# Optimization experiments

Measured on AMD Instinct MI355X. Metric: run time of the kernel, lower is better.

Reference implementation:

```python
import jax, jax.numpy as jnp
import numpy as np

S, B, V = 128, 64, 32000
EH, EO, H, O = 512, 512, 1024, 1024
THRESH = 1e-06


def _thresh(x):
    # nn.Threshold(1e-6, 0): x if x > 1e-6 else 0
    return jnp.where(x > THRESH, x, 0.0)


def setup_inputs() -> dict:
    key = jax.random.key(0)
    ks = jax.random.split(key, 12)
    ids = jax.random.randint(ks[0], (S, B), 0, V, dtype=jnp.int32)
    s = 0.02
    return {
        "ids": ids,
        "W1": jax.random.normal(ks[1], (EH, V), jnp.float32) * s,
        "b1": jax.random.normal(ks[2], (EH,), jnp.float32) * s,
        "W2": jax.random.normal(ks[3], (EO, EH), jnp.float32) * s,
        "b2": jax.random.normal(ks[4], (EO,), jnp.float32) * s,
        "W_ih": jax.random.normal(ks[5], (3 * H, EO), jnp.float32) * s,
        "b_ih": jax.random.normal(ks[6], (3 * H,), jnp.float32) * s,
        "W_hh": jax.random.normal(ks[7], (3 * H, H), jnp.float32) * s,
        "b_hh": jax.random.normal(ks[8], (3 * H,), jnp.float32) * s,
        "W_out": jax.random.normal(ks[9], (O, H), jnp.float32) * s,
        "b_out": jax.random.normal(ks[10], (O,), jnp.float32) * s,
    }


def reference(ids, W1, b1, W2, b2, W_ih, b_ih, W_hh, b_hh, W_out, b_out):
    # one_hot(ids, V) @ W1.T + b1 == exact gather of W1 columns (sum of zeros is exact)
    emb = _thresh(jnp.take(W1.T, ids, axis=0) + b1)            # [S, B, EH]
    x = _thresh(jnp.einsum('sbe,oe->sbo', emb, W2) + b2)       # [S, B, EO]
    # Precompute all input-gate projections in one GEMM
    xW = jnp.einsum('sbe,ge->sbg', x, W_ih) + b_ih             # [S, B, 3H]

    def step(h, xw):
        gh = h @ W_hh.T + b_hh                                 # [B, 3H]
        xr, xz, xn = jnp.split(xw, 3, axis=-1)
        hr, hz, hn = jnp.split(gh, 3, axis=-1)
        r = jax.nn.sigmoid(xr + hr)
        z = jax.nn.sigmoid(xz + hz)
        n = jnp.tanh(xn + r * hn)
        h_new = (1.0 - z) * n + z * h
        return h_new, None

    h0 = jnp.zeros((B, H), dtype=x.dtype)
    hT, _ = jax.lax.scan(step, h0, xW)                         # [B, H]
    # Dropout is identity in inference; final Linear
    out = hT @ W_out.T + b_out                                 # [B, O]
    return out[None]                                           # [1, B, O] (h_n layout)
```

## Files before the change

### kernel.cpp

```cpp
#include <hip/hip_runtime.h>
#include <stdint.h>
#include <stddef.h>

#define S_LEN 128
#define B_SZ  64
#define V_SZ  32000
#define EH    512
#define EO    512
#define H_SZ  1024
#define O_SZ  1024
#define G3    3072

typedef __attribute__((ext_vector_type(8))) short short8;
typedef __attribute__((ext_vector_type(4))) float floatx4;
typedef __attribute__((ext_vector_type(8))) unsigned short ushortx8;
typedef __attribute__((ext_vector_type(4))) unsigned uintx4;

__device__ __forceinline__ unsigned short f2bf(float f) {
  unsigned u = __builtin_bit_cast(unsigned, f);
  u += 0x7FFFu + ((u >> 16) & 1u);
  return (unsigned short)(u >> 16);
}
__device__ __forceinline__ float bf2f(unsigned short h) {
  unsigned u = ((unsigned)h) << 16;
  return __builtin_bit_cast(float, u);
}

__device__ __forceinline__ void gld_lds16(const void* g, void* l) {
  __builtin_amdgcn_global_load_lds((const __attribute__((address_space(1))) void*)g,
                                   (__attribute__((address_space(3))) void*)l, 16, 0, 0);
}

__global__ __launch_bounds__(256) void cvt2_bf16(const float* __restrict__ a,
                                                 const float* __restrict__ b,
                                                 unsigned short* __restrict__ out) {
  const int na4 = (EO * EH) / 4;
  int i = blockIdx.x * 256 + threadIdx.x;
  const float* src;
  int off;
  if (i < na4) { src = a; off = i; }
  else         { src = b; off = i - na4; }
  float4 v = ((const float4*)src)[off];
  ushort4 o;
  o.x = f2bf(v.x); o.y = f2bf(v.y); o.z = f2bf(v.z); o.w = f2bf(v.w);
  ((ushort4*)out)[i] = o;
}

__global__ __launch_bounds__(256) void transpose_w1_bf16(const float* __restrict__ W1,
                                                         unsigned short* __restrict__ W1T) {
  __shared__ unsigned short tile[64][72];
  int t = threadIdx.x;
  int v0 = blockIdx.x * 64;
  int e0 = blockIdx.y * 64;
  for (int i = 0; i < 4; ++i) {
    int e = (t >> 4) + i * 16;
    int v = (t & 15) * 4;
    float4 w = *(const float4*)&W1[(size_t)(e0 + e) * V_SZ + v0 + v];
    tile[v + 0][e] = f2bf(w.x);
    tile[v + 1][e] = f2bf(w.y);
    tile[v + 2][e] = f2bf(w.z);
    tile[v + 3][e] = f2bf(w.w);
  }
  __syncthreads();
  for (int i = 0; i < 2; ++i) {
    int v = (t >> 3) + i * 32;
    int e = (t & 7) * 8;
    ushortx8 o;
    for (int j = 0; j < 8; ++j) o[j] = tile[v][e + j];
    *(ushortx8*)&W1T[(size_t)(v0 + v) * EH + e0 + e] = o;
  }
}

__global__ __launch_bounds__(256) void gather_emb(const int* __restrict__ ids,
                                                  const unsigned short* __restrict__ W1T,
                                                  const float* __restrict__ b1,
                                                  unsigned short* __restrict__ emb) {
  int t = threadIdx.x;
  int tok = blockIdx.x * 4 + (t >> 6);
  int lane = t & 63;
  int id = ids[tok];
  ushortx8 w = *(const ushortx8*)&W1T[(size_t)id * EH + lane * 8];
  float4 blo = *(const float4*)&b1[lane * 8];
  float4 bhi = *(const float4*)&b1[lane * 8 + 4];
  float bv[8] = {blo.x, blo.y, blo.z, blo.w, bhi.x, bhi.y, bhi.z, bhi.w};
  ushortx8 o;
  for (int j = 0; j < 8; ++j) {
    float x = bf2f(w[j]) + bv[j];
    x = (x > 1e-6f) ? x : 0.0f;
    o[j] = f2bf(x);
  }
  *(ushortx8*)&emb[(size_t)tok * EH + lane * 8] = o;
}

template <int ACT, int OUT_BF16>
__global__ __launch_bounds__(256) void gemm_bt(const unsigned short* __restrict__ A,
                                               const unsigned short* __restrict__ B,
                                               const float* __restrict__ bias,
                                               void* __restrict__ Cout,
                                               int M, int N, int K) {
  __shared__ unsigned short lA[128 * 64];
  __shared__ unsigned short lB[128 * 64];
  int t = threadIdx.x;
  int lane = t & 63;
  int wave = t >> 6;
  int bn = blockIdx.x, bm = blockIdx.y;
  int wm = (wave >> 1) * 64;
  int wn = (wave & 1) * 64;
  floatx4 acc[4][4] = {};

  int srow = t >> 3;
  int sslot = (t & 7) ^ (srow & 7);
  int scol = sslot * 8;

  const unsigned short* aptr[4];
  const unsigned short* bptr[4];
#pragma unroll
  for (int p = 0; p < 4; ++p) {
    int gra = bm * 128 + p * 32 + srow;  if (gra >= M) gra = M - 1;
    aptr[p] = A + (size_t)gra * K + scol;
    bptr[p] = B + (size_t)(bn * 128 + p * 32 + srow) * K + scol;
  }

  for (int k0 = 0; k0 < K; k0 += 64) {
    __syncthreads();
#pragma unroll
    for (int p = 0; p < 4; ++p) {
      gld_lds16(aptr[p] + k0, &lA[p * 2048 + t * 8]);
      gld_lds16(bptr[p] + k0, &lB[p * 2048 + t * 8]);
    }
    __syncthreads();
#pragma unroll
    for (int kk = 0; kk < 2; ++kk) {
      short8 af[4], bfr[4];
#pragma unroll
      for (int i = 0; i < 4; ++i) {
        int row = wm + i * 16 + (lane & 15);
        int phys = (kk * 4 + (lane >> 4)) ^ (row & 7);
        af[i] = *(const short8*)&lA[row * 64 + phys * 8];
      }
#pragma unroll
      for (int j = 0; j < 4; ++j) {
        int row = wn + j * 16 + (lane & 15);
        int phys = (kk * 4 + (lane >> 4)) ^ (row & 7);
        bfr[j] = *(const short8*)&lB[row * 64 + phys * 8];
      }
#pragma unroll
      for (int i = 0; i < 4; ++i)
#pragma unroll
        for (int j = 0; j < 4; ++j)
          acc[i][j] = __builtin_amdgcn_mfma_f32_16x16x32_bf16(af[i], bfr[j], acc[i][j], 0, 0, 0);
    }
  }

  int rowq = (lane >> 4) * 4;
  for (int j = 0; j < 4; ++j) {
    int col = bn * 128 + wn + j * 16 + (lane & 15);
    float bv = bias[col];
    for (int i = 0; i < 4; ++i) {
      int row0 = bm * 128 + wm + i * 16 + rowq;
      for (int r = 0; r < 4; ++r) {
        int row = row0 + r;
        if (row < M) {
          float v = acc[i][j][r] + bv;
          if (ACT) v = (v > 1e-6f) ? v : 0.0f;
          if (OUT_BF16) ((unsigned short*)Cout)[(size_t)row * N + col] = f2bf(v);
          else          ((float*)Cout)[(size_t)row * N + col] = v;
        }
      }
    }
  }
}

__global__ __launch_bounds__(256) void prep_whh(const float* __restrict__ W_hh,
                                                unsigned short* __restrict__ Wprep) {
  int tid = blockIdx.x * 256 + threadIdx.x;
  int lane = tid & 63;
  int c = tid >> 6;
  int cg = c / 96;
  int r  = c % 96;
  int g  = r >> 5;
  int t  = r & 31;
  int row = g * H_SZ + cg * 16 + (lane & 15);
  int k   = t * 32 + (lane >> 4) * 8;
  const float* src = &W_hh[(size_t)row * H_SZ + k];
  float4 v0 = *(const float4*)src;
  float4 v1 = *(const float4*)(src + 4);
  ushortx8 o;
  o[0] = f2bf(v0.x); o[1] = f2bf(v0.y); o[2] = f2bf(v0.z); o[3] = f2bf(v0.w);
  o[4] = f2bf(v1.x); o[5] = f2bf(v1.y); o[6] = f2bf(v1.z); o[7] = f2bf(v1.w);
  ((ushortx8*)Wprep)[tid] = o;
}

__global__ __launch_bounds__(256) void prep_wih(const float* __restrict__ W_ih,
                                                unsigned short* __restrict__ Wihp) {
  int tid = blockIdx.x * 256 + threadIdx.x;
  int lane = tid & 63;
  int c = tid >> 6;
  int cg = c / 48;
  int r  = c % 48;
  int g  = r >> 4;
  int kq = r & 15;
  int row = g * H_SZ + cg * 16 + (lane & 15);
  int k   = kq * 32 + (lane >> 4) * 8;
  const float* src = &W_ih[(size_t)row * EO + k];
  float4 v0 = *(const float4*)src;
  float4 v1 = *(const float4*)(src + 4);
  ushortx8 o;
  o[0] = f2bf(v0.x); o[1] = f2bf(v0.y); o[2] = f2bf(v0.z); o[3] = f2bf(v0.w);
  o[4] = f2bf(v1.x); o[5] = f2bf(v1.y); o[6] = f2bf(v1.z); o[7] = f2bf(v1.w);
  ((ushortx8*)Wihp)[tid] = o;
}

__global__ __launch_bounds__(256, 1) void gru_persist(const unsigned short* __restrict__ hprep0,
                                                      unsigned short* __restrict__ hprep1,
                                                      unsigned short* __restrict__ hbfinal,
                                                      const unsigned short* __restrict__ Wprep,
                                                      const unsigned short* __restrict__ Wihp,
                                                      const float* __restrict__ b_hh,
                                                      const float* __restrict__ b_ih,
                                                      const unsigned short* __restrict__ x,
                                                      unsigned* __restrict__ bar) {
  __shared__ unsigned short lB[96 * 512];
  __shared__ unsigned short lWih[48 * 512];
  __shared__ float lgh[3][4][256];
  __shared__ float lgxn[4][256];
  int t = threadIdx.x;
  int lane = t & 63;
  int w = t >> 6;
  int bg = blockIdx.x >> 6;
  int cg = blockIdx.x & 63;

  const unsigned short* wsrc = Wprep + (size_t)cg * 96 * 512;
  for (int i = 0; i < 24; ++i) {
    int c = w * 24 + i;
    gld_lds16(wsrc + (size_t)c * 512 + lane * 8, &lB[c * 512 + lane * 8]);
  }
  const unsigned short* wxs = Wihp + (size_t)cg * 48 * 512;
  for (int i = 0; i < 12; ++i) {
    int c = w * 12 + i;
    gld_lds16(wxs + (size_t)c * 512 + lane * 8, &lWih[c * 512 + lane * 8]);
  }

  int b_loc = t >> 4;
  int j_loc = t & 15;
  int jcol = cg * 16 + j_loc;
  int bglob = bg * 16 + b_loc;
  float brz_r = b_hh[jcol] + b_ih[jcol];
  float brz_z = b_hh[H_SZ + jcol] + b_ih[H_SZ + jcol];
  float bhn  = b_hh[2 * H_SZ + jcol];
  float bihn = b_ih[2 * H_SZ + jcol];
  int tt2 = jcol >> 5;
  int q   = (jcol >> 3) & 3;
  int jj  = jcol & 7;
  int Ls  = b_loc | (q << 4);
  size_t hw_off32 = ((((size_t)(bg * 32 + tt2) * 64 + Ls) * 8) + (jj & ~1)) >> 1;

  const unsigned short* hbufs[2] = {hprep0, hprep1};
  unsigned* barp = bar + bg * 64;
  float hmaster = 0.0f;

  const unsigned short* xbase =
      x + ((size_t)(bg * 16 + (lane & 15))) * EO + (lane >> 4) * 8 + (w * 4) * 32;

  __syncthreads();

  uintx4 xf[4];
#pragma unroll
  for (int i = 0; i < 4; ++i)
    asm volatile("global_load_dwordx4 %0, %1, off" : "=v"(xf[i]) : "v"(xbase + i * 32));

  for (int s = 0; s < S_LEN; ++s) {
    const unsigned short* hr = hbufs[s & 1];
    unsigned* hw32 = (unsigned*)hbufs[(s + 1) & 1];

    uintx4 av[8];
#pragma unroll
    for (int i = 0; i < 8; ++i) {
      int tt = w * 8 + i;
      const void* ap = hr + ((size_t)(bg * 32 + tt) * 64 + lane) * 8;
      asm volatile("global_load_dwordx4 %0, %1, off sc1" : "=v"(av[i]) : "v"(ap));
    }
    asm volatile("s_waitcnt vmcnt(0)"
                 : "+v"(av[0]), "+v"(av[1]), "+v"(av[2]), "+v"(av[3]),
                   "+v"(av[4]), "+v"(av[5]), "+v"(av[6]), "+v"(av[7]),
                   "+v"(xf[0]), "+v"(xf[1]), "+v"(xf[2]), "+v"(xf[3])
                 :: "memory");

    floatx4 acc[3] = {};
    floatx4 accn = {};
#pragma unroll
    for (int i = 0; i < 8; ++i) {
      int tt = w * 8 + i;
      short8 a = __builtin_bit_cast(short8, av[i]);
#pragma unroll
      for (int g = 0; g < 3; ++g) {
        short8 bfr = *(const short8*)&lB[((g * 32 + tt) * 64 + lane) * 8];
        acc[g] = __builtin_amdgcn_mfma_f32_16x16x32_bf16(a, bfr, acc[g], 0, 0, 0);
      }
    }
#pragma unroll
    for (int i = 0; i < 4; ++i) {
      int kq = w * 4 + i;
      short8 a = __builtin_bit_cast(short8, xf[i]);
      short8 b0 = *(const short8*)&lWih[((0 * 16 + kq) * 64 + lane) * 8];
      short8 b1 = *(const short8*)&lWih[((1 * 16 + kq) * 64 + lane) * 8];
      short8 b2 = *(const short8*)&lWih[((2 * 16 + kq) * 64 + lane) * 8];
      acc[0] = __builtin_amdgcn_mfma_f32_16x16x32_bf16(a, b0, acc[0], 0, 0, 0);
      acc[1] = __builtin_amdgcn_mfma_f32_16x16x32_bf16(a, b1, acc[1], 0, 0, 0);
      accn   = __builtin_amdgcn_mfma_f32_16x16x32_bf16(a, b2, accn,   0, 0, 0);
    }

    if (s + 1 < S_LEN) {
      const unsigned short* xrow = xbase + (size_t)(s + 1) * B_SZ * EO;
#pragma unroll
      for (int i = 0; i < 4; ++i)
        asm volatile("global_load_dwordx4 %0, %1, off" : "=v"(xf[i]) : "v"(xrow + i * 32));
    }

#pragma unroll
    for (int g = 0; g < 3; ++g)
#pragma unroll
      for (int r = 0; r < 4; ++r)
        lgh[g][w][((lane >> 4) * 4 + r) * 16 + (lane & 15)] = acc[g][r];
#pragma unroll
    for (int r = 0; r < 4; ++r)
      lgxn[w][((lane >> 4) * 4 + r) * 16 + (lane & 15)] = accn[r];
    __syncthreads();

    float grs = lgh[0][0][t] + lgh[0][1][t] + lgh[0][2][t] + lgh[0][3][t] + brz_r;
    float gzs = lgh[1][0][t] + lgh[1][1][t] + lgh[1][2][t] + lgh[1][3][t] + brz_z;
    float ghn = lgh[2][0][t] + lgh[2][1][t] + lgh[2][2][t] + lgh[2][3][t] + bhn;
    float xnv = lgxn[0][t] + lgxn[1][t] + lgxn[2][t] + lgxn[3][t] + bihn;
    float rr = 1.0f / (1.0f + __expf(-grs));
    float zz = 1.0f / (1.0f + __expf(-gzs));
    float nn = tanhf(xnv + rr * ghn);
    float hnew = (1.0f - zz) * nn + zz * hmaster;
    hmaster = hnew;

    unsigned hb = (unsigned)f2bf(hnew);
    unsigned other = (unsigned)__shfl_xor((int)hb, 1);
    if ((jj & 1) == 0) {
      unsigned packed = hb | (other << 16);
      __hip_atomic_store(hw32 + hw_off32, packed,
                         __ATOMIC_RELAXED, __HIP_MEMORY_SCOPE_AGENT);
    }
    if (s == S_LEN - 1) hbfinal[(size_t)bglob * H_SZ + jcol] = (unsigned short)hb;

    if (s < S_LEN - 1) {
      __syncthreads();
      if (t == 0) {
        __hip_atomic_fetch_add(barp, 1u, __ATOMIC_RELAXED, __HIP_MEMORY_SCOPE_AGENT);
        unsigned target = 64u * (unsigned)(s + 1);
        while (__hip_atomic_load(barp, __ATOMIC_RELAXED, __HIP_MEMORY_SCOPE_AGENT) < target)
          __builtin_amdgcn_s_sleep(2);
      }
      __syncthreads();
    }
  }
}

extern "C" void kernel_launch(void* const* d_in, const int* in_sizes, int n_in,
                              void* d_out, int out_size, void* d_ws, size_t ws_size,
                              hipStream_t stream) {
  const int*   ids   = (const int*)d_in[0];
  const float* W1    = (const float*)d_in[1];
  const float* b1    = (const float*)d_in[2];
  const float* W2    = (const float*)d_in[3];
  const float* b2    = (const float*)d_in[4];
  const float* W_ih  = (const float*)d_in[5];
  const float* b_ih  = (const float*)d_in[6];
  const float* W_hh  = (const float*)d_in[7];
  const float* b_hh  = (const float*)d_in[8];
  const float* W_out = (const float*)d_in[9];
  const float* b_out = (const float*)d_in[10];
  float* out = (float*)d_out;

  uint8_t* wsp = (uint8_t*)d_ws;
  auto alloc = [&](size_t bytes) {
    uint8_t* p = wsp;
    wsp += (bytes + 255) & ~(size_t)255;
    return p;
  };
  unsigned short* W1T   = (unsigned short*)alloc((size_t)V_SZ * EH * 2);
  unsigned short* W2b   = (unsigned short*)alloc((size_t)EO * EH * 2);
  unsigned short* Woutb = (unsigned short*)alloc((size_t)O_SZ * H_SZ * 2);
  unsigned short* Wprep = (unsigned short*)alloc((size_t)G3 * H_SZ * 2);
  unsigned short* Wihp  = (unsigned short*)alloc((size_t)G3 * EO * 2);
  unsigned short* emb   = (unsigned short*)alloc((size_t)S_LEN * B_SZ * EH * 2);
  unsigned short* x     = (unsigned short*)alloc((size_t)S_LEN * B_SZ * EO * 2);
  unsigned short* hprep0 = (unsigned short*)alloc((size_t)B_SZ * H_SZ * 2);
  unsigned short* hprep1 = (unsigned short*)alloc((size_t)B_SZ * H_SZ * 2);
  unsigned short* hbfinal = (unsigned short*)alloc((size_t)B_SZ * H_SZ * 2);
  unsigned*       bar     = (unsigned*)alloc(1024);

  cvt2_bf16<<<dim3(1280), 256, 0, stream>>>(W2, W_out, W2b);

  prep_whh<<<dim3(1536), 256, 0, stream>>>(W_hh, Wprep);
  prep_wih<<<dim3(768), 256, 0, stream>>>(W_ih, Wihp);

  hipMemsetAsync(hprep0, 0, (size_t)B_SZ * H_SZ * 2, stream);
  hipMemsetAsync(bar, 0, 1024, stream);

  transpose_w1_bf16<<<dim3(V_SZ / 64, EH / 64), 256, 0, stream>>>(W1, W1T);

  gather_emb<<<dim3(S_LEN * B_SZ / 4), 256, 0, stream>>>(ids, W1T, b1, emb);

  gemm_bt<1, 1><<<dim3(EO / 128, S_LEN * B_SZ / 128), 256, 0, stream>>>(
      emb, W2b, b2, x, S_LEN * B_SZ, EO, EH);

  {
    void* args[] = {(void*)&hprep0, (void*)&hprep1, (void*)&hbfinal,
                    (void*)&Wprep, (void*)&Wihp, (void*)&b_hh, (void*)&b_ih,
                    (void*)&x, (void*)&bar};
    hipLaunchCooperativeKernel((const void*)gru_persist, dim3(256), dim3(256),
                               args, 0, stream);
  }

  gemm_bt<0, 0><<<dim3(O_SZ / 128, 1), 256, 0, stream>>>(
      hbfinal, Woutb, b_out, out, B_SZ, O_SZ, H_SZ);
}
```

Before: 621.0 us.

## Fuse weight prep kernels and fold output projection into persistent GRU kernel

Merges the W2/W_hh/W_ih/W_out bf16 conversion kernels and the barrier memset into a single prep launch. The initial hidden-state memset is replaced by zeroing the h operand at step 0. The final output Linear is computed inside the persistent GRU kernel after one extra grid barrier, reusing LDS for a pre-laid-out W_out tile, which removes the trailing GEMM launch. The intent is to cut launch count and the small, poorly parallel final GEMM, at the cost of one more barrier and extra LDS loads at the end of the recurrence.

```diff
diff --git a/kernel.cpp b/kernel.cpp
--- a/kernel.cpp
+++ b/kernel.cpp
@@ -31,19 +31,63 @@
                                    (__attribute__((address_space(3))) void*)l, 16, 0, 0);
 }
 
-__global__ __launch_bounds__(256) void cvt2_bf16(const float* __restrict__ a,
-                                                 const float* __restrict__ b,
-                                                 unsigned short* __restrict__ out) {
-  const int na4 = (EO * EH) / 4;
-  int i = blockIdx.x * 256 + threadIdx.x;
+__global__ __launch_bounds__(256) void prep_all(const float* __restrict__ W2,
+                                                const float* __restrict__ W_hh,
+                                                const float* __restrict__ W_ih,
+                                                const float* __restrict__ W_out,
+                                                unsigned short* __restrict__ W2b,
+                                                unsigned short* __restrict__ Wprep,
+                                                unsigned short* __restrict__ Wihp,
+                                                unsigned short* __restrict__ Woutp,
+                                                unsigned* __restrict__ bar) {
+  int b = blockIdx.x;
+  int t = threadIdx.x;
+  if (b < 256) {
+    int i = b * 256 + t;
+    float4 v = ((const float4*)W2)[i];
+    ushort4 o;
+    o.x = f2bf(v.x); o.y = f2bf(v.y); o.z = f2bf(v.z); o.w = f2bf(v.w);
+    ((ushort4*)W2b)[i] = o;
+    if (b == 0) bar[t] = 0;
+    return;
+  }
+  int lane, row, k;
   const float* src;
-  int off;
-  if (i < na4) { src = a; off = i; }
-  else         { src = b; off = i - na4; }
-  float4 v = ((const float4*)src)[off];
-  ushort4 o;
-  o.x = f2bf(v.x); o.y = f2bf(v.y); o.z = f2bf(v.z); o.w = f2bf(v.w);
-  ((ushort4*)out)[i] = o;
+  ushortx8* dst;
+  if (b < 256 + 1536) {
+    int tid = (b - 256) * 256 + t;
+    lane = tid & 63;
+    int c = tid >> 6;
+    int cg = c / 96, r = c % 96, g = r >> 5, tt = r & 31;
+    row = g * H_SZ + cg * 16 + (lane & 15);
+    k   = tt * 32 + (lane >> 4) * 8;
+    src = &W_hh[(size_t)row * H_SZ + k];
+    dst = (ushortx8*)Wprep + tid;
+  } else if (b < 256 + 1536 + 768) {
+    int tid = (b - 1792) * 256 + t;
+    lane = tid & 63;
+    int c = tid >> 6;
+    int cg = c / 48, r = c % 48, g = r >> 4, kq = r & 15;
+    row = g * H_SZ + cg * 16 + (lane & 15);
+    k   = kq * 32 + (lane >> 4) * 8;
+    src = &W_ih[(size_t)row * EO + k];
+    dst = (ushortx8*)Wihp + tid;
+  } else {
+    int tid = (b - 2560) * 256 + t;
+    lane = tid & 63;
+    int c = tid >> 6;
+    int cg = c >> 5, kq = c & 31;
+    row = cg * 16 + (lane & 15);
+    k   = kq * 32 + (lane >> 4) * 8;
+    src = &W_out[(size_t)row * H_SZ + k];
+    dst = (ushortx8*)Woutp + tid;
+  }
+  float4 v0 = *(const float4*)src;
+  float4 v1 = *(const float4*)(src + 4);
+  ushortx8 o;
+  o[0] = f2bf(v0.x); o[1] = f2bf(v0.y); o[2] = f2bf(v0.z); o[3] = f2bf(v0.w);
+  o[4] = f2bf(v1.x); o[5] = f2bf(v1.y); o[6] = f2bf(v1.z); o[7] = f2bf(v1.w);
+  *dst = o;
 }
 
 __global__ __launch_bounds__(256) void transpose_w1_bf16(const float* __restrict__ W1,
@@ -171,54 +215,17 @@
   }
 }
 
-__global__ __launch_bounds__(256) void prep_whh(const float* __restrict__ W_hh,
-                                                unsigned short* __restrict__ Wprep) {
-  int tid = blockIdx.x * 256 + threadIdx.x;
-  int lane = tid & 63;
-  int c = tid >> 6;
-  int cg = c / 96;
-  int r  = c % 96;
-  int g  = r >> 5;
-  int t  = r & 31;
-  int row = g * H_SZ + cg * 16 + (lane & 15);
-  int k   = t * 32 + (lane >> 4) * 8;
-  const float* src = &W_hh[(size_t)row * H_SZ + k];
-  float4 v0 = *(const float4*)src;
-  float4 v1 = *(const float4*)(src + 4);
-  ushortx8 o;
-  o[0] = f2bf(v0.x); o[1] = f2bf(v0.y); o[2] = f2bf(v0.z); o[3] = f2bf(v0.w);
-  o[4] = f2bf(v1.x); o[5] = f2bf(v1.y); o[6] = f2bf(v1.z); o[7] = f2bf(v1.w);
-  ((ushortx8*)Wprep)[tid] = o;
-}
-
-__global__ __launch_bounds__(256) void prep_wih(const float* __restrict__ W_ih,
-                                                unsigned short* __restrict__ Wihp) {
-  int tid = blockIdx.x * 256 + threadIdx.x;
-  int lane = tid & 63;
-  int c = tid >> 6;
-  int cg = c / 48;
-  int r  = c % 48;
-  int g  = r >> 4;
-  int kq = r & 15;
-  int row = g * H_SZ + cg * 16 + (lane & 15);
-  int k   = kq * 32 + (lane >> 4) * 8;
-  const float* src = &W_ih[(size_t)row * EO + k];
-  float4 v0 = *(const float4*)src;
-  float4 v1 = *(const float4*)(src + 4);
-  ushortx8 o;
-  o[0] = f2bf(v0.x); o[1] = f2bf(v0.y); o[2] = f2bf(v0.z); o[3] = f2bf(v0.w);
-  o[4] = f2bf(v1.x); o[5] = f2bf(v1.y); o[6] = f2bf(v1.z); o[7] = f2bf(v1.w);
-  ((ushortx8*)Wihp)[tid] = o;
-}
-
 __global__ __launch_bounds__(256, 1) void gru_persist(const unsigned short* __restrict__ hprep0,
                                                       unsigned short* __restrict__ hprep1,
                                                       unsigned short* __restrict__ hbfinal,
                                                       const unsigned short* __restrict__ Wprep,
                                                       const unsigned short* __restrict__ Wihp,
+                                                      const unsigned short* __restrict__ Woutp,
                                                       const float* __restrict__ b_hh,
                                                       const float* __restrict__ b_ih,
+                                                      const float* __restrict__ b_out,
                                                       const unsigned short* __restrict__ x,
+                                                      float* __restrict__ out,
                                                       unsigned* __restrict__ bar) {
   __shared__ unsigned short lB[96 * 512];
   __shared__ unsigned short lWih[48 * 512];
@@ -274,11 +281,16 @@
     unsigned* hw32 = (unsigned*)hbufs[(s + 1) & 1];
 
     uintx4 av[8];
-#pragma unroll
-    for (int i = 0; i < 8; ++i) {
-      int tt = w * 8 + i;
-      const void* ap = hr + ((size_t)(bg * 32 + tt) * 64 + lane) * 8;
-      asm volatile("global_load_dwordx4 %0, %1, off sc1" : "=v"(av[i]) : "v"(ap));
+    if (s == 0) {
+#pragma unroll
+      for (int i = 0; i < 8; ++i) av[i] = (uintx4){0u, 0u, 0u, 0u};
+    } else {
+#pragma unroll
+      for (int i = 0; i < 8; ++i) {
+        int tt = w * 8 + i;
+        const void* ap = hr + ((size_t)(bg * 32 + tt) * 64 + lane) * 8;
+        asm volatile("global_load_dwordx4 %0, %1, off sc1" : "=v"(av[i]) : "v"(ap));
+      }
     }
     asm volatile("s_waitcnt vmcnt(0)"
                  : "+v"(av[0]), "+v"(av[1]), "+v"(av[2]), "+v"(av[3]),
@@ -343,19 +355,56 @@
       unsigned packed = hb | (other << 16);
       __hip_atomic_store(hw32 + hw_off32, packed,
                          __ATOMIC_RELAXED, __HIP_MEMORY_SCOPE_AGENT);
-    }
-    if (s == S_LEN - 1) hbfinal[(size_t)bglob * H_SZ + jcol] = (unsigned short)hb;
-
-    if (s < S_LEN - 1) {
-      __syncthreads();
-      if (t == 0) {
-        __hip_atomic_fetch_add(barp, 1u, __ATOMIC_RELAXED, __HIP_MEMORY_SCOPE_AGENT);
-        unsigned target = 64u * (unsigned)(s + 1);
-        while (__hip_atomic_load(barp, __ATOMIC_RELAXED, __HIP_MEMORY_SCOPE_AGENT) < target)
-          __builtin_amdgcn_s_sleep(2);
-      }
-      __syncthreads();
-    }
+      if (s == S_LEN - 1) {
+        __hip_atomic_store((unsigned*)hbfinal + (((size_t)bglob * H_SZ + jcol) >> 1),
+                           packed, __ATOMIC_RELAXED, __HIP_MEMORY_SCOPE_AGENT);
+      }
+    }
+
+    __syncthreads();
+    if (t == 0) {
+      __hip_atomic_fetch_add(barp, 1u, __ATOMIC_RELAXED, __HIP_MEMORY_SCOPE_AGENT);
+      unsigned target = 64u * (unsigned)(s + 1);
+      while (__hip_atomic_load(barp, __ATOMIC_RELAXED, __HIP_MEMORY_SCOPE_AGENT) < target)
+        __builtin_amdgcn_s_sleep(2);
+    }
+    __syncthreads();
+  }
+
+  {
+    const unsigned short* wos = Woutp + (size_t)cg * 32 * 512;
+#pragma unroll
+    for (int i = 0; i < 8; ++i) {
+      int c = w * 8 + i;
+      gld_lds16(wos + (size_t)c * 512 + lane * 8, &lB[c * 512 + lane * 8]);
+    }
+    uintx4 hv[8];
+#pragma unroll
+    for (int i = 0; i < 8; ++i) {
+      int kq = w * 8 + i;
+      const void* hp = hbfinal + (size_t)(bg * 16 + (lane & 15)) * H_SZ +
+                       kq * 32 + (lane >> 4) * 8;
+      asm volatile("global_load_dwordx4 %0, %1, off sc1" : "=v"(hv[i]) : "v"(hp));
+    }
+    __syncthreads();
+    asm volatile("s_waitcnt vmcnt(0)"
+                 : "+v"(hv[0]), "+v"(hv[1]), "+v"(hv[2]), "+v"(hv[3]),
+                   "+v"(hv[4]), "+v"(hv[5]), "+v"(hv[6]), "+v"(hv[7])
+                 :: "memory");
+    floatx4 acco = {};
+#pragma unroll
+    for (int i = 0; i < 8; ++i) {
+      int kq = w * 8 + i;
+      short8 a = __builtin_bit_cast(short8, hv[i]);
+      short8 bfr = *(const short8*)&lB[kq * 512 + lane * 8];
+      acco = __builtin_amdgcn_mfma_f32_16x16x32_bf16(a, bfr, acco, 0, 0, 0);
+    }
+#pragma unroll
+    for (int r = 0; r < 4; ++r)
+      lgh[0][w][((lane >> 4) * 4 + r) * 16 + (lane & 15)] = acco[r];
+    __syncthreads();
+    float o = lgh[0][0][t] + lgh[0][1][t] + lgh[0][2][t] + lgh[0][3][t] + b_out[jcol];
+    out[(size_t)bglob * O_SZ + jcol] = o;
   }
 }
 
@@ -383,9 +432,9 @@
   };
   unsigned short* W1T   = (unsigned short*)alloc((size_t)V_SZ * EH * 2);
   unsigned short* W2b   = (unsigned short*)alloc((size_t)EO * EH * 2);
-  unsigned short* Woutb = (unsigned short*)alloc((size_t)O_SZ * H_SZ * 2);
   unsigned short* Wprep = (unsigned short*)alloc((size_t)G3 * H_SZ * 2);
   unsigned short* Wihp  = (unsigned short*)alloc((size_t)G3 * EO * 2);
+  unsigned short* Woutp = (unsigned short*)alloc((size_t)O_SZ * H_SZ * 2);
   unsigned short* emb   = (unsigned short*)alloc((size_t)S_LEN * B_SZ * EH * 2);
   unsigned short* x     = (unsigned short*)alloc((size_t)S_LEN * B_SZ * EO * 2);
   unsigned short* hprep0 = (unsigned short*)alloc((size_t)B_SZ * H_SZ * 2);
@@ -393,13 +442,8 @@
   unsigned short* hbfinal = (unsigned short*)alloc((size_t)B_SZ * H_SZ * 2);
   unsigned*       bar     = (unsigned*)alloc(1024);
 
-  cvt2_bf16<<<dim3(1280), 256, 0, stream>>>(W2, W_out, W2b);
-
-  prep_whh<<<dim3(1536), 256, 0, stream>>>(W_hh, Wprep);
-  prep_wih<<<dim3(768), 256, 0, stream>>>(W_ih, Wihp);
-
-  hipMemsetAsync(hprep0, 0, (size_t)B_SZ * H_SZ * 2, stream);
-  hipMemsetAsync(bar, 0, 1024, stream);
+  prep_all<<<dim3(3072), 256, 0, stream>>>(W2, W_hh, W_ih, W_out,
+                                           W2b, Wprep, Wihp, Woutp, bar);
 
   transpose_w1_bf16<<<dim3(V_SZ / 64, EH / 64), 256, 0, stream>>>(W1, W1T);
 
@@ -410,12 +454,10 @@
 
   {
     void* args[] = {(void*)&hprep0, (void*)&hprep1, (void*)&hbfinal,
-                    (void*)&Wprep, (void*)&Wihp, (void*)&b_hh, (void*)&b_ih,
-                    (void*)&x, (void*)&bar};
+                    (void*)&Wprep, (void*)&Wihp, (void*)&Woutp,
+                    (void*)&b_hh, (void*)&b_ih, (void*)&b_out,
+                    (void*)&x, (void*)&out, (void*)&bar};
     hipLaunchCooperativeKernel((const void*)gru_persist, dim3(256), dim3(256),
                                args, 0, stream);
   }
-
-  gemm_bt<0, 0><<<dim3(O_SZ / 128, 1), 256, 0, stream>>>(
-      hbfinal, Woutb, b_out, out, B_SZ, O_SZ, H_SZ);
-}
+}
```

Result: faster. 591.6 us (-4.7%).
